# Optimization experiments

Hardware: AMD Instinct MI355X
Metric: run time of the kernel (lower is better)

The kernel has to match this reference:

```python
import jax, jax.numpy as jnp
import numpy as np

B, H, NC, BETA = 8192, 1024, 3, 1.0


def setup_inputs() -> dict:
    key = jax.random.key(0)
    ks = jax.random.split(key, 24)
    u = 1.0 / np.sqrt(2 * H)  # torch default Linear init bound for fan_in=2H

    def W(k):
        return jax.random.uniform(k, (H, 2 * H), minval=-u, maxval=u, dtype=jnp.float32)

    def b(k):
        return jax.random.uniform(k, (H,), minval=-u, maxval=u, dtype=jnp.float32)

    decay_bound = np.sqrt(3) / np.sqrt(2 * H)  # custom_init for layer_decay
    inp = {
        "x_i": jax.random.normal(ks[0], (B, H), dtype=jnp.float32),
        "hidden_i_minus": jax.random.normal(ks[1], (B, H), dtype=jnp.float32),
        "cell_i_minus": jax.random.normal(ks[2], (B, H), dtype=jnp.float32),
        "cell_bar_i_minus": jax.random.normal(ks[3], (B, H), dtype=jnp.float32),
        "W_input": W(ks[4]), "b_input": b(ks[5]),
        "W_forget": W(ks[6]), "b_forget": b(ks[7]),
        "W_output": W(ks[8]), "b_output": b(ks[9]),
        "W_input_bar": W(ks[10]), "b_input_bar": b(ks[11]),
        "W_forget_bar": W(ks[12]), "b_forget_bar": b(ks[13]),
        "W_pre_c": W(ks[14]), "b_pre_c": b(ks[15]),
        "W_decay": jax.random.uniform(ks[16], (H * (NC + 1), 2 * H), minval=0.0, maxval=decay_bound, dtype=jnp.float32),
        "b_decay": jnp.zeros((H * (NC + 1),), dtype=jnp.float32),
    }
    return inp


def reference(x_i, hidden_i_minus, cell_i_minus, cell_bar_i_minus,
              W_input, b_input, W_forget, b_forget, W_output, b_output,
              W_input_bar, b_input_bar, W_forget_bar, b_forget_bar,
              W_pre_c, b_pre_c, W_decay, b_decay):
    xh = jnp.concatenate([x_i, hidden_i_minus], axis=1)  # [B, 2H]
    # Fuse the 7 linear layers into a single GEMM.
    Wcat = jnp.concatenate([W_input, W_forget, W_output, W_input_bar,
                            W_forget_bar, W_pre_c, W_decay], axis=0)  # [10H, 2H]
    bcat = jnp.concatenate([b_input, b_forget, b_output, b_input_bar,
                            b_forget_bar, b_pre_c, b_decay], axis=0)
    z = xh @ Wcat.T + bcat  # [B, 6H + (NC+1)H]
    gi = jax.nn.sigmoid(z[:, 0 * H:1 * H])
    gf = jax.nn.sigmoid(z[:, 1 * H:2 * H])
    go = jax.nn.sigmoid(z[:, 2 * H:3 * H])
    gib = jax.nn.sigmoid(z[:, 3 * H:4 * H])
    gfb = jax.nn.sigmoid(z[:, 4 * H:5 * H])
    pre_c = jnp.tanh(z[:, 5 * H:6 * H])
    gate_decay = (jax.nn.softplus(BETA * z[:, 6 * H:]) / BETA).reshape(-1, H, NC + 1)
    cell_i = gf * cell_i_minus + gi * pre_c
    cell_bar_i = gfb * cell_bar_i_minus + gib * pre_c
    return (cell_i, cell_bar_i, gate_decay, go)
```

## Files before the change

### kernel.cpp

```cpp
#include <hip/hip_runtime.h>
#include <hip/hip_bf16.h>
#include <cstdint>
#include <cmath>

#define B_DIM 8192
#define H_DIM 1024
#define K_DIM 2048
#define N_DIM 10240

typedef __bf16 bf16x8 __attribute__((ext_vector_type(8)));
typedef float  f32x4  __attribute__((ext_vector_type(4)));

static __device__ __forceinline__ float sigmoid_f(float z) {
    return 1.0f / (1.0f + __expf(-z));
}
static __device__ __forceinline__ float tanh_f(float z) {
    return 1.0f - 2.0f / (1.0f + __expf(2.0f * z));
}
static __device__ __forceinline__ float softplus_f(float z) {
    return fmaxf(z, 0.0f) + log1pf(__expf(-fabsf(z)));
}

static __device__ __forceinline__ void store_bf16x4(__bf16* p, float4 v) {
    alignas(8) __bf16 t[4] = {(__bf16)v.x, (__bf16)v.y, (__bf16)v.z, (__bf16)v.w};
    *reinterpret_cast<uint2*>(p) = *reinterpret_cast<const uint2*>(t);
}

static __device__ __forceinline__ void gload_lds16(const void* g, void* l) {
    auto* gp = reinterpret_cast<__attribute__((address_space(1))) unsigned int*>(
        reinterpret_cast<uintptr_t>(g));
    auto* lp = reinterpret_cast<__attribute__((address_space(3))) unsigned int*>(
        reinterpret_cast<uintptr_t>(l));
    __builtin_amdgcn_global_load_lds(gp, lp, 16, 0, 0);
}


__global__ void pack_xh_kernel(const float* __restrict__ x, const float* __restrict__ h,
                               __bf16* __restrict__ xh) {
    const int64_t total = (int64_t)B_DIM * K_DIM / 4;
    for (int64_t i = (int64_t)blockIdx.x * blockDim.x + threadIdx.x; i < total;
         i += (int64_t)gridDim.x * blockDim.x) {
        int64_t e = i << 2;
        int64_t b = e >> 11;
        int     c = (int)(e & 2047);
        const float* src = (c < H_DIM) ? (x + b * H_DIM + c) : (h + b * H_DIM + (c - H_DIM));
        float4 v = *reinterpret_cast<const float4*>(src);
        store_bf16x4(xh + e, v);
    }
}

__global__ void pack_W_kernel(const float* __restrict__ w0, const float* __restrict__ w1,
                              const float* __restrict__ w2, const float* __restrict__ w3,
                              const float* __restrict__ w4, const float* __restrict__ w5,
                              const float* __restrict__ wd, __bf16* __restrict__ dst) {
    const int64_t total = (int64_t)N_DIM * K_DIM / 4;
    for (int64_t i = (int64_t)blockIdx.x * blockDim.x + threadIdx.x; i < total;
         i += (int64_t)gridDim.x * blockDim.x) {
        int64_t e   = i << 2;
        int     blk = (int)(e >> 21);
        const float* src;
        int64_t off;
        if (blk < 6) {
            src = (blk == 0) ? w0 : (blk == 1) ? w1 : (blk == 2) ? w2
                : (blk == 3) ? w3 : (blk == 4) ? w4 : w5;
            off = e - ((int64_t)blk << 21);
        } else {
            src = wd;
            off = e - ((int64_t)6 << 21);
        }
        float4 v = *reinterpret_cast<const float4*>(src + off);
        store_bf16x4(dst + e, v);
    }
}

__global__ void pack_bias_kernel(const float* __restrict__ b0, const float* __restrict__ b1,
                                 const float* __restrict__ b2, const float* __restrict__ b3,
                                 const float* __restrict__ b4, const float* __restrict__ b5,
                                 const float* __restrict__ bd, float* __restrict__ dst) {
    int i = blockIdx.x * blockDim.x + threadIdx.x;
    if (i >= N_DIM) return;
    int blk = i >> 10;
    float v;
    if (blk < 6) {
        const float* s = (blk == 0) ? b0 : (blk == 1) ? b1 : (blk == 2) ? b2
                       : (blk == 3) ? b3 : (blk == 4) ? b4 : b5;
        v = s[i - (blk << 10)];
    } else {
        v = bd[i - (6 << 10)];
    }
    dst[i] = v;
}


#define MFMA_(Af, Bf, C) __builtin_amdgcn_mfma_f32_16x16x32_bf16(Af, Bf, C, 0, 0, 0)

#define ACCS(F) \
    F(0,0) F(0,1) F(0,2) F(0,3) F(1,0) F(1,1) F(1,2) F(1,3) \
    F(2,0) F(2,1) F(2,2) F(2,3) F(3,0) F(3,1) F(3,2) F(3,3)

#define READA(KH) \
    a0 = ldA(0, KH); a1 = ldA(1, KH); a2 = ldA(2, KH); a3 = ldA(3, KH);

#define MFMA_COL(N, KH) { \
    bf16x8 bb = ldB(N, KH); \
    c0##N = MFMA_(a0, bb, c0##N); c1##N = MFMA_(a1, bb, c1##N); \
    c2##N = MFMA_(a2, bb, c2##N); c3##N = MFMA_(a3, bb, c3##N); }

__global__ __launch_bounds__(256, 5) void gemm_fused(
    const __bf16* __restrict__ A,
    const __bf16* __restrict__ W,
    const float* __restrict__ bias,
    float* __restrict__ out,
    __bf16* __restrict__ ggi, __bf16* __restrict__ ggf,
    __bf16* __restrict__ ggib, __bf16* __restrict__ ggfb,
    __bf16* __restrict__ gpc) {
    __shared__ __bf16 As[8192];
    __shared__ __bf16 Bs[8192];

    const int bid = blockIdx.x;
    const int xcd = bid & 7;
    const int j   = bid >> 3;
    const int ch  = j / 80;
    const int jj  = j % 80;
    const int tm  = (xcd << 3) + (jj & 7);
    const int tn  = ch * 10 + (jj >> 3);

    const int t     = threadIdx.x;
    const int lane  = t & 63;
    const int w     = t >> 6;
    const int wmOff = (w >> 1) << 6;
    const int wnOff = (w & 1) << 6;
    const int lr    = lane & 15;
    const int kg    = lane >> 4;

    const int64_t Arow0 = (int64_t)tm * 128;
    const int64_t Wrow0 = (int64_t)tn * 128;

#define DA(M, N) f32x4 c##M##N = {0.f, 0.f, 0.f, 0.f};
    ACCS(DA)
#undef DA
    bf16x8 a0, a1, a2, a3;

    const int srcChunk = ((t & 7) ^ ((t >> 3) & 7)) << 3;
    const __bf16* aSrc = A + (Arow0 + (t >> 3)) * (int64_t)K_DIM + srcChunk;
    const __bf16* bSrc = W + (Wrow0 + (t >> 3)) * (int64_t)K_DIM + srcChunk;
    __bf16* ldsA = As + t * 8;
    __bf16* ldsB = Bs + t * 8;

    const int xr  = lr & 7;
    const int ca  = kg ^ xr;
    const char* aRd0 = reinterpret_cast<const char*>(As) + (wmOff + lr) * 128 + (ca << 4);
    const char* aRd1 = reinterpret_cast<const char*>(As) + (wmOff + lr) * 128 + ((ca ^ 4) << 4);
    const char* bRd0 = reinterpret_cast<const char*>(Bs) + (wnOff + lr) * 128 + (ca << 4);
    const char* bRd1 = reinterpret_cast<const char*>(Bs) + (wnOff + lr) * 128 + ((ca ^ 4) << 4);

    auto ldA = [&](int m, int kh) {
        return *reinterpret_cast<const bf16x8*>((kh ? aRd1 : aRd0) + m * 2048);
    };
    auto ldB = [&](int n, int kh) {
        return *reinterpret_cast<const bf16x8*>((kh ? bRd1 : bRd0) + n * 2048);
    };

#pragma unroll 1
    for (int kt = 0; kt < 32; ++kt) {
        const int k0 = kt << 6;
        __syncthreads();
        gload_lds16(aSrc + 0 * (32 * K_DIM) + k0, ldsA + 0 * 2048);
        gload_lds16(aSrc + 1 * (32 * K_DIM) + k0, ldsA + 1 * 2048);
        gload_lds16(aSrc + 2 * (32 * K_DIM) + k0, ldsA + 2 * 2048);
        gload_lds16(aSrc + 3 * (32 * K_DIM) + k0, ldsA + 3 * 2048);
        gload_lds16(bSrc + 0 * (32 * K_DIM) + k0, ldsB + 0 * 2048);
        gload_lds16(bSrc + 1 * (32 * K_DIM) + k0, ldsB + 1 * 2048);
        gload_lds16(bSrc + 2 * (32 * K_DIM) + k0, ldsB + 2 * 2048);
        gload_lds16(bSrc + 3 * (32 * K_DIM) + k0, ldsB + 3 * 2048);
        __syncthreads();
        READA(0)
        MFMA_COL(0, 0) MFMA_COL(1, 0) MFMA_COL(2, 0) MFMA_COL(3, 0)
        READA(1)
        MFMA_COL(0, 1) MFMA_COL(1, 1) MFMA_COL(2, 1) MFMA_COL(3, 1)
    }
    __syncthreads();

    const float bv0 = bias[Wrow0 + wnOff + 0 * 16 + lr];
    const float bv1 = bias[Wrow0 + wnOff + 1 * 16 + lr];
    const float bv2 = bias[Wrow0 + wnOff + 2 * 16 + lr];
    const float bv3 = bias[Wrow0 + wnOff + 3 * 16 + lr];

    const int     blk = tn >> 3;
    const int     lg  = lane >> 4;
    const int64_t BH  = (int64_t)B_DIM * H_DIM;

    auto epi = [&](int m, int n, f32x4 a, float bv) {
        const int64_t rowb = Arow0 + wmOff + m * 16 + lg * 4;
        const int     colo = wnOff + n * 16 + lr;
        if (blk == 2) {
            float* dst = out + 6 * BH + (Wrow0 - 2 * (int64_t)H_DIM) + colo;
#pragma unroll
            for (int r = 0; r < 4; ++r)
                __builtin_nontemporal_store(sigmoid_f(a[r] + bv), dst + (rowb + r) * H_DIM);
        } else if (blk >= 6) {
            float* dst = out + 2 * BH + (Wrow0 - 6 * (int64_t)H_DIM) + colo;
#pragma unroll
            for (int r = 0; r < 4; ++r)
                __builtin_nontemporal_store(softplus_f(a[r] + bv), dst + (rowb + r) * 4 * H_DIM);
        } else {
            __bf16* gp = (blk == 0) ? ggi : (blk == 1) ? ggf
                       : (blk == 3) ? ggib : (blk == 4) ? ggfb : gpc;
            __bf16* dst = gp + (int)(Wrow0 & 1023) + colo;
            if (blk == 5) {
#pragma unroll
                for (int r = 0; r < 4; ++r) dst[(rowb + r) * H_DIM] = (__bf16)tanh_f(a[r] + bv);
            } else {
#pragma unroll
                for (int r = 0; r < 4; ++r) dst[(rowb + r) * H_DIM] = (__bf16)sigmoid_f(a[r] + bv);
            }
        }
    };
#define EPI(M, N) epi(M, N, c##M##N, bv##N);
    ACCS(EPI)
#undef EPI
}


__global__ void combine_kernel(const __bf16* __restrict__ ggi, const __bf16* __restrict__ ggf,
                               const __bf16* __restrict__ ggib, const __bf16* __restrict__ ggfb,
                               const __bf16* __restrict__ gpc, const float* __restrict__ cp,
                               const float* __restrict__ cbp, float* __restrict__ out) {
    const int64_t BH    = (int64_t)B_DIM * H_DIM;
    const int64_t total = BH / 8;
    for (int64_t i = (int64_t)blockIdx.x * blockDim.x + threadIdx.x; i < total;
         i += (int64_t)gridDim.x * blockDim.x) {
        int64_t e = i << 3;
        bf16x8 vgi  = *reinterpret_cast<const bf16x8*>(ggi + e);
        bf16x8 vgf  = *reinterpret_cast<const bf16x8*>(ggf + e);
        bf16x8 vgib = *reinterpret_cast<const bf16x8*>(ggib + e);
        bf16x8 vgfb = *reinterpret_cast<const bf16x8*>(ggfb + e);
        bf16x8 vpc  = *reinterpret_cast<const bf16x8*>(gpc + e);
        float4 c0  = *reinterpret_cast<const float4*>(cp + e);
        float4 c1  = *reinterpret_cast<const float4*>(cp + e + 4);
        float4 cb0 = *reinterpret_cast<const float4*>(cbp + e);
        float4 cb1 = *reinterpret_cast<const float4*>(cbp + e + 4);
        float cpa[8] = {c0.x, c0.y, c0.z, c0.w, c1.x, c1.y, c1.z, c1.w};
        float cba[8] = {cb0.x, cb0.y, cb0.z, cb0.w, cb1.x, cb1.y, cb1.z, cb1.w};
        float ci[8], cbi[8];
#pragma unroll
        for (int j = 0; j < 8; ++j) {
            float pc = (float)vpc[j];
            ci[j]  = (float)vgf[j]  * cpa[j] + (float)vgi[j]  * pc;
            cbi[j] = (float)vgfb[j] * cba[j] + (float)vgib[j] * pc;
        }
        f32x4 ci0 = {ci[0], ci[1], ci[2], ci[3]};
        f32x4 ci1 = {ci[4], ci[5], ci[6], ci[7]};
        f32x4 cb0v = {cbi[0], cbi[1], cbi[2], cbi[3]};
        f32x4 cb1v = {cbi[4], cbi[5], cbi[6], cbi[7]};
        f32x4* o0 = reinterpret_cast<f32x4*>(out + e);
        __builtin_nontemporal_store(ci0, &o0[0]);
        __builtin_nontemporal_store(ci1, &o0[1]);
        f32x4* o1 = reinterpret_cast<f32x4*>(out + BH + e);
        __builtin_nontemporal_store(cb0v, &o1[0]);
        __builtin_nontemporal_store(cb1v, &o1[1]);
    }
}


extern "C" void kernel_launch(void* const* d_in, const int* in_sizes, int n_in,
                              void* d_out, int out_size, void* d_ws, size_t ws_size,
                              hipStream_t stream) {
    const float* x   = (const float*)d_in[0];
    const float* h   = (const float*)d_in[1];
    const float* cp  = (const float*)d_in[2];
    const float* cbp = (const float*)d_in[3];
    const float* Wi  = (const float*)d_in[4];
    const float* bi  = (const float*)d_in[5];
    const float* Wf  = (const float*)d_in[6];
    const float* bfo = (const float*)d_in[7];
    const float* Wo  = (const float*)d_in[8];
    const float* bo  = (const float*)d_in[9];
    const float* Wib = (const float*)d_in[10];
    const float* bib = (const float*)d_in[11];
    const float* Wfb = (const float*)d_in[12];
    const float* bfb = (const float*)d_in[13];
    const float* Wpc = (const float*)d_in[14];
    const float* bpc = (const float*)d_in[15];
    const float* Wd  = (const float*)d_in[16];
    const float* bd  = (const float*)d_in[17];
    float* out = (float*)d_out;

    char* ws = (char*)d_ws;
    __bf16* xh   = (__bf16*)ws;
    __bf16* Wb   = (__bf16*)(ws + 33554432);
    float*  bias = (float*)(ws + 75497472);
    __bf16* ggi  = (__bf16*)(ws + 75538432);
    const size_t BH = (size_t)B_DIM * H_DIM;
    __bf16* ggf  = ggi + BH;
    __bf16* ggib = ggf + BH;
    __bf16* ggfb = ggib + BH;
    __bf16* gpc  = ggfb + BH;

    pack_xh_kernel<<<2048, 256, 0, stream>>>(x, h, xh);
    pack_W_kernel<<<2048, 256, 0, stream>>>(Wi, Wf, Wo, Wib, Wfb, Wpc, Wd, Wb);
    pack_bias_kernel<<<40, 256, 0, stream>>>(bi, bfo, bo, bib, bfb, bpc, bd, bias);

    const int grid = (B_DIM / 128) * (N_DIM / 128);
    gemm_fused<<<grid, 256, 0, stream>>>(xh, Wb, bias, out, ggi, ggf, ggib, ggfb, gpc);

    combine_kernel<<<4096, 256, 0, stream>>>(ggi, ggf, ggib, ggfb, gpc, cp, cbp, out);
}
```

Before: 464.7 us.

## Double-buffer LDS tiles with K=32 stages to overlap loads and MFMA

Splits the shared-memory A/B tiles into two buffers of K=32 each and restructures the main loop so the global-to-LDS copy of the next stage is issued before computing the current one. This leaves one barrier per stage and is meant to hide global load latency behind MFMA work. The swizzle and read addressing change to match the 64-byte row layout, and launch bounds drop from 5 to 4 blocks per SM. The final iteration issues a redundant wrap-around prefetch, and correctness depends on the async LDS loads being complete at each barrier.

```diff
diff --git a/kernel.cpp b/kernel.cpp
--- a/kernel.cpp
+++ b/kernel.cpp
@@ -98,15 +98,22 @@
     F(0,0) F(0,1) F(0,2) F(0,3) F(1,0) F(1,1) F(1,2) F(1,3) \
     F(2,0) F(2,1) F(2,2) F(2,3) F(3,0) F(3,1) F(3,2) F(3,3)
 
-#define READA(KH) \
-    a0 = ldA(0, KH); a1 = ldA(1, KH); a2 = ldA(2, KH); a3 = ldA(3, KH);
-
-#define MFMA_COL(N, KH) { \
-    bf16x8 bb = ldB(N, KH); \
+#define MFMA_COL(BUF, N) { \
+    bf16x8 bb = ldB(BUF, N); \
     c0##N = MFMA_(a0, bb, c0##N); c1##N = MFMA_(a1, bb, c1##N); \
     c2##N = MFMA_(a2, bb, c2##N); c3##N = MFMA_(a3, bb, c3##N); }
 
-__global__ __launch_bounds__(256, 5) void gemm_fused(
+#define COMPUTE(BUF) \
+    a0 = ldA(BUF, 0); a1 = ldA(BUF, 1); a2 = ldA(BUF, 2); a3 = ldA(BUF, 3); \
+    MFMA_COL(BUF, 0) MFMA_COL(BUF, 1) MFMA_COL(BUF, 2) MFMA_COL(BUF, 3)
+
+#define STAGE(BUF, K0) \
+    gload_lds16(aSrc + (K0),               ldsA + (BUF) * 4096); \
+    gload_lds16(aSrc + 64 * K_DIM + (K0),  ldsA + (BUF) * 4096 + 2048); \
+    gload_lds16(bSrc + (K0),               ldsB + (BUF) * 4096); \
+    gload_lds16(bSrc + 64 * K_DIM + (K0),  ldsB + (BUF) * 4096 + 2048);
+
+__global__ __launch_bounds__(256, 4) void gemm_fused(
     const __bf16* __restrict__ A,
     const __bf16* __restrict__ W,
     const float* __restrict__ bias,
@@ -114,8 +121,8 @@
     __bf16* __restrict__ ggi, __bf16* __restrict__ ggf,
     __bf16* __restrict__ ggib, __bf16* __restrict__ ggfb,
     __bf16* __restrict__ gpc) {
-    __shared__ __bf16 As[8192];
-    __shared__ __bf16 Bs[8192];
+    __shared__ __bf16 As[2 * 4096];
+    __shared__ __bf16 Bs[2 * 4096];
 
     const int bid = blockIdx.x;
     const int xcd = bid & 7;
@@ -141,45 +148,35 @@
 #undef DA
     bf16x8 a0, a1, a2, a3;
 
-    const int srcChunk = ((t & 7) ^ ((t >> 3) & 7)) << 3;
-    const __bf16* aSrc = A + (Arow0 + (t >> 3)) * (int64_t)K_DIM + srcChunk;
-    const __bf16* bSrc = W + (Wrow0 + (t >> 3)) * (int64_t)K_DIM + srcChunk;
+    const int srcChunk = ((t & 3) ^ ((t >> 3) & 3)) << 3;
+    const __bf16* aSrc = A + (Arow0 + (t >> 2)) * (int64_t)K_DIM + srcChunk;
+    const __bf16* bSrc = W + (Wrow0 + (t >> 2)) * (int64_t)K_DIM + srcChunk;
     __bf16* ldsA = As + t * 8;
     __bf16* ldsB = Bs + t * 8;
 
-    const int xr  = lr & 7;
-    const int ca  = kg ^ xr;
-    const char* aRd0 = reinterpret_cast<const char*>(As) + (wmOff + lr) * 128 + (ca << 4);
-    const char* aRd1 = reinterpret_cast<const char*>(As) + (wmOff + lr) * 128 + ((ca ^ 4) << 4);
-    const char* bRd0 = reinterpret_cast<const char*>(Bs) + (wnOff + lr) * 128 + (ca << 4);
-    const char* bRd1 = reinterpret_cast<const char*>(Bs) + (wnOff + lr) * 128 + ((ca ^ 4) << 4);
-
-    auto ldA = [&](int m, int kh) {
-        return *reinterpret_cast<const bf16x8*>((kh ? aRd1 : aRd0) + m * 2048);
+    const int cs = kg ^ ((lr >> 1) & 3);
+    const char* aRd = reinterpret_cast<const char*>(As) + (wmOff + lr) * 64 + (cs << 4);
+    const char* bRd = reinterpret_cast<const char*>(Bs) + (wnOff + lr) * 64 + (cs << 4);
+
+    auto ldA = [&](int buf, int m) {
+        return *reinterpret_cast<const bf16x8*>(aRd + buf * 8192 + m * 1024);
     };
-    auto ldB = [&](int n, int kh) {
-        return *reinterpret_cast<const bf16x8*>((kh ? bRd1 : bRd0) + n * 2048);
+    auto ldB = [&](int buf, int n) {
+        return *reinterpret_cast<const bf16x8*>(bRd + buf * 8192 + n * 1024);
     };
 
+    STAGE(0, 0)
+    __syncthreads();
+
 #pragma unroll 1
-    for (int kt = 0; kt < 32; ++kt) {
-        const int k0 = kt << 6;
+    for (int kt = 0; kt < 64; kt += 2) {
+        STAGE(1, (kt + 1) << 5)
+        COMPUTE(0)
         __syncthreads();
-        gload_lds16(aSrc + 0 * (32 * K_DIM) + k0, ldsA + 0 * 2048);
-        gload_lds16(aSrc + 1 * (32 * K_DIM) + k0, ldsA + 1 * 2048);
-        gload_lds16(aSrc + 2 * (32 * K_DIM) + k0, ldsA + 2 * 2048);
-        gload_lds16(aSrc + 3 * (32 * K_DIM) + k0, ldsA + 3 * 2048);
-        gload_lds16(bSrc + 0 * (32 * K_DIM) + k0, ldsB + 0 * 2048);
-        gload_lds16(bSrc + 1 * (32 * K_DIM) + k0, ldsB + 1 * 2048);
-        gload_lds16(bSrc + 2 * (32 * K_DIM) + k0, ldsB + 2 * 2048);
-        gload_lds16(bSrc + 3 * (32 * K_DIM) + k0, ldsB + 3 * 2048);
+        STAGE(0, ((kt + 2) & 63) << 5)
+        COMPUTE(1)
         __syncthreads();
-        READA(0)
-        MFMA_COL(0, 0) MFMA_COL(1, 0) MFMA_COL(2, 0) MFMA_COL(3, 0)
-        READA(1)
-        MFMA_COL(0, 1) MFMA_COL(1, 1) MFMA_COL(2, 1) MFMA_COL(3, 1)
-    }
-    __syncthreads();
+    }
 
     const float bv0 = bias[Wrow0 + wnOff + 0 * 16 + lr];
     const float bv1 = bias[Wrow0 + wnOff + 1 * 16 + lr];
```

Measured after the change: 528.6 us. 13.8% more time.
